# Performance work log

Measured on AMD Instinct MI355X. Metric: run time of the kernel, lower is better.

The kernel has to match this reference:

```python
import jax, jax.numpy as jnp
import numpy as np


def _quant(x, bits):
    # Symmetric per-tensor uniform quantization with straight-through rounding
    # (scale detached, as in typical QConv2d/QLinear low-bit implementations).
    n = 2.0 ** (bits - 1) - 1.0  # 7 levels each side for 4-bit
    s = jax.lax.stop_gradient(jnp.max(jnp.abs(x)) / n + 1e-8)
    q = jnp.clip(x / s, -n, n)
    q = q + jax.lax.stop_gradient(jnp.round(q) - q)  # STE round
    return q * s


def setup_inputs() -> dict:
    key = jax.random.key(0)
    k1, k2, k3, k4, k5 = jax.random.split(key, 5)
    B = 8192
    x = jax.random.normal(k1, (B, 1, 28, 28), dtype=jnp.float32)
    conv_w = jax.random.normal(k2, (16, 1, 3, 3), dtype=jnp.float32) * 0.1
    conv_b = jax.random.normal(k3, (16,), dtype=jnp.float32) * 0.01
    fc_w = jax.random.normal(k4, (10, 576), dtype=jnp.float32) * 0.05
    fc_b = jax.random.normal(k5, (10,), dtype=jnp.float32) * 0.01
    return {"x": x, "conv_w": conv_w, "conv_b": conv_b, "fc_w": fc_w, "fc_b": fc_b}


def reference(x, conv_w, conv_b, fc_w, fc_b):
    WBIT = 4
    ABIT = 4
    # QConv2d: quantize activations and weights to 4-bit, then conv (VALID, stride 1)
    xq = _quant(x, ABIT)
    wq = _quant(conv_w, WBIT)
    y = jax.lax.conv_general_dilated(
        xq, wq, window_strides=(1, 1), padding="VALID",
        dimension_numbers=("NCHW", "OIHW", "NCHW"))  # [B,16,26,26]
    y = y + conv_b[None, :, None, None]
    y = jax.nn.relu(y)
    # MaxPool2d(4): 4x4 window, stride 4 -> [B,16,6,6]
    y = jax.lax.reduce_window(y, -jnp.inf, jax.lax.max,
                              (1, 1, 4, 4), (1, 1, 4, 4), "VALID")
    flat = y.reshape(y.shape[0], -1)  # [B,576], channel-major like torch.flatten
    # QLinear: quantize activations and weights, then matmul
    fq = _quant(flat, ABIT)
    fwq = _quant(fc_w, WBIT)
    out = fq @ fwq.T + fc_b  # [B,10]
    return out
```

## Files before the change

kernel.cpp:

```cpp
#include <hip/hip_runtime.h>


#define DEV __device__ __forceinline__

DEV float quantq(float v, float s) {
  return rintf(fminf(7.0f, fmaxf(-7.0f, v / s)));
}

DEV float block_reduce_max(float v, float* smem) {
#pragma unroll
  for (int off = 32; off > 0; off >>= 1)
    v = fmaxf(v, __shfl_xor(v, off, 64));
  __syncthreads();
  if ((threadIdx.x & 63) == 0) smem[threadIdx.x >> 6] = v;
  __syncthreads();
  float m = smem[0];
  for (int i = 1; i < ((int)blockDim.x >> 6); ++i) m = fmaxf(m, smem[i]);
  return m;
}

__global__ __launch_bounds__(256) void prep_kernel(
    const float* __restrict__ cw, const float* __restrict__ fw,
    unsigned int* __restrict__ scal) {
  __shared__ float smem[8];
  const int tid = threadIdx.x;
  float m1 = 0.f;
  for (int i = tid; i < 144; i += 256) m1 = fmaxf(m1, fabsf(cw[i]));
  m1 = block_reduce_max(m1, smem);
  float m2 = 0.f;
  for (int i = tid; i < 5760; i += 256) m2 = fmaxf(m2, fabsf(fw[i]));
  m2 = block_reduce_max(m2, smem);
  if (tid == 0) {
    scal[0] = 0u;
    scal[1] = __float_as_uint(m1);
    scal[2] = __float_as_uint(m2);
    scal[3] = 0u;
  }
}

__global__ __launch_bounds__(256) void maxabs_x_kernel(
    const float4* __restrict__ x4, int n4, unsigned int* __restrict__ scal) {
  __shared__ float smem[8];
  float m = 0.f;
  for (int i = blockIdx.x * blockDim.x + threadIdx.x; i < n4;
       i += gridDim.x * blockDim.x) {
    float4 v = x4[i];
    m = fmaxf(m, fmaxf(fmaxf(fabsf(v.x), fabsf(v.y)),
                       fmaxf(fabsf(v.z), fabsf(v.w))));
  }
  m = block_reduce_max(m, smem);
  if (threadIdx.x == 0) atomicMax(scal + 0, __float_as_uint(m));
}

#define IMGS_PER_BLK 7
__global__ __launch_bounds__(256) void conv_pool_kernel(
    const float* __restrict__ x, const float* __restrict__ cw,
    const float* __restrict__ cb, unsigned int* __restrict__ scal,
    float* __restrict__ flat) {
  __shared__ __align__(16) float qx[IMGS_PER_BLK * 784];
  __shared__ float qw[16][9];
  __shared__ float bias[16];
  __shared__ float smem[8];
  const int tid = threadIdx.x;
  const int b0 = blockIdx.x * IMGS_PER_BLK;
  const int nimg = min(IMGS_PER_BLK, 8192 - b0);
  const float sx = __uint_as_float(scal[0]) / 7.0f + 1e-8f;
  const float sw = __uint_as_float(scal[1]) / 7.0f + 1e-8f;
  const float sxw = sx * sw;
  {
    const float4* x4 = (const float4*)x + b0 * 196;
    float4* q4 = (float4*)qx;
    const int n4 = nimg * 196;
    for (int i = tid; i < n4; i += 256) {
      float4 v = x4[i];
      float4 q;
      q.x = quantq(v.x, sx); q.y = quantq(v.y, sx);
      q.z = quantq(v.z, sx); q.w = quantq(v.w, sx);
      q4[i] = q;
    }
  }
  if (tid < 144) qw[tid / 9][tid % 9] = quantq(cw[tid], sw);
  if (tid < 16) bias[tid] = cb[tid];
  __syncthreads();
  float lmax = 0.f;
  if (tid < nimg * 36) {
    const int img = tid / 36, pp = tid % 36, pi = pp / 6, pj = pp % 6;
    const float* base = &qx[img * 784 + pi * 4 * 28 + pj * 4];
    float r[36];
#pragma unroll
    for (int rr = 0; rr < 6; ++rr)
#pragma unroll
      for (int cc = 0; cc < 6; ++cc) r[rr * 6 + cc] = base[rr * 28 + cc];
    float* fo = &flat[(b0 + img) * 576 + pp];
#pragma unroll
    for (int c = 0; c < 16; ++c) {
      const float w0 = qw[c][0], w1 = qw[c][1], w2 = qw[c][2];
      const float w3 = qw[c][3], w4 = qw[c][4], w5 = qw[c][5];
      const float w6 = qw[c][6], w7 = qw[c][7], w8 = qw[c][8];
      const float bc = bias[c];
      float m = 0.f;
#pragma unroll
      for (int dr = 0; dr < 4; ++dr)
#pragma unroll
        for (int dc = 0; dc < 4; ++dc) {
          const float* q = &r[dr * 6 + dc];
          float acc = q[0] * w0 + q[1] * w1 + q[2] * w2
                    + q[6] * w3 + q[7] * w4 + q[8] * w5
                    + q[12] * w6 + q[13] * w7 + q[14] * w8;
          m = fmaxf(m, acc * sxw + bc);
        }
      fo[c * 36] = m;
      lmax = fmaxf(lmax, m);
    }
  }
  lmax = block_reduce_max(lmax, smem);
  if (tid == 0) atomicMax(scal + 3, __float_as_uint(lmax));
}

__global__ __launch_bounds__(256) void fc_kernel(
    const float* __restrict__ flat, const float* __restrict__ fw,
    const float* __restrict__ fb, const unsigned int* __restrict__ scal,
    float* __restrict__ out) {
  __shared__ float qfw[5760];
  __shared__ float sb[10];
  const float sf = __uint_as_float(scal[3]) / 7.0f + 1e-8f;
  const float sfw = __uint_as_float(scal[2]) / 7.0f + 1e-8f;
  const int tid = threadIdx.x;
  for (int i = tid; i < 5760; i += 256) qfw[i] = quantq(fw[i], sfw);
  if (tid < 10) sb[tid] = fb[tid];
  __syncthreads();
  const int wave = tid >> 6, lane = tid & 63;
  const int b = blockIdx.x * 4 + wave;
  float acc[10];
#pragma unroll
  for (int o = 0; o < 10; ++o) acc[o] = 0.f;
  const float* frow = &flat[b * 576];
#pragma unroll
  for (int j = 0; j < 9; ++j) {
    const int k = j * 64 + lane;
    const float qf = quantq(frow[k], sf);
#pragma unroll
    for (int o = 0; o < 10; ++o) acc[o] += qf * qfw[o * 576 + k];
  }
#pragma unroll
  for (int o = 0; o < 10; ++o)
#pragma unroll
    for (int off = 32; off > 0; off >>= 1)
      acc[o] += __shfl_xor(acc[o], off, 64);
  if (lane == 0) {
    const float ss = sf * sfw;
#pragma unroll
    for (int o = 0; o < 10; ++o) out[b * 10 + o] = acc[o] * ss + sb[o];
  }
}

extern "C" void kernel_launch(void* const* d_in, const int* in_sizes, int n_in,
                              void* d_out, int out_size, void* d_ws, size_t ws_size,
                              hipStream_t stream) {
  const float* x  = (const float*)d_in[0];
  const float* cw = (const float*)d_in[1];
  const float* cb = (const float*)d_in[2];
  const float* fw = (const float*)d_in[3];
  const float* fb = (const float*)d_in[4];
  float* out = (float*)d_out;
  unsigned int* scal = (unsigned int*)d_ws;
  float* flat = (float*)((char*)d_ws + 256);

  prep_kernel<<<1, 256, 0, stream>>>(cw, fw, scal);
  maxabs_x_kernel<<<1024, 256, 0, stream>>>(
      (const float4*)x, (8192 * 784) / 4, scal);
  conv_pool_kernel<<<(8192 + IMGS_PER_BLK - 1) / IMGS_PER_BLK, 256, 0, stream>>>(
      x, cw, cb, scal, flat);
  fc_kernel<<<2048, 256, 0, stream>>>(flat, fw, fb, scal, out);
}
```

Before: 157.0 us.

## Fold weight max-abs into x reduction and parallelize conv over channels

Removes the separate single-block prep kernel by folding the conv and fc weight max-abs reductions into block 0 of the input max-abs kernel, with a memset to zero the scalars instead. The conv-pool kernel now processes one image per 576-thread block, one thread per (channel, pooled pixel), rather than 7 images per block with 36 threads looping over 16 channels. This aims to raise thread-level parallelism and coalesce the flat stores, at the cost of reloading input rows per channel from shared memory and more block scheduling overhead.

```diff
diff --git a/kernel.cpp b/kernel.cpp
--- a/kernel.cpp
+++ b/kernel.cpp
@@ -19,27 +19,9 @@
   return m;
 }
 
-__global__ __launch_bounds__(256) void prep_kernel(
-    const float* __restrict__ cw, const float* __restrict__ fw,
-    unsigned int* __restrict__ scal) {
-  __shared__ float smem[8];
-  const int tid = threadIdx.x;
-  float m1 = 0.f;
-  for (int i = tid; i < 144; i += 256) m1 = fmaxf(m1, fabsf(cw[i]));
-  m1 = block_reduce_max(m1, smem);
-  float m2 = 0.f;
-  for (int i = tid; i < 5760; i += 256) m2 = fmaxf(m2, fabsf(fw[i]));
-  m2 = block_reduce_max(m2, smem);
-  if (tid == 0) {
-    scal[0] = 0u;
-    scal[1] = __float_as_uint(m1);
-    scal[2] = __float_as_uint(m2);
-    scal[3] = 0u;
-  }
-}
-
-__global__ __launch_bounds__(256) void maxabs_x_kernel(
-    const float4* __restrict__ x4, int n4, unsigned int* __restrict__ scal) {
+__global__ __launch_bounds__(256) void maxabs_kernel(
+    const float4* __restrict__ x4, int n4, const float* __restrict__ cw,
+    const float* __restrict__ fw, unsigned int* __restrict__ scal) {
   __shared__ float smem[8];
   float m = 0.f;
   for (int i = blockIdx.x * blockDim.x + threadIdx.x; i < n4;
@@ -50,70 +32,74 @@
   }
   m = block_reduce_max(m, smem);
   if (threadIdx.x == 0) atomicMax(scal + 0, __float_as_uint(m));
+  if (blockIdx.x == 0) {
+    const int tid = threadIdx.x;
+    float m1 = 0.f;
+    for (int i = tid; i < 144; i += 256) m1 = fmaxf(m1, fabsf(cw[i]));
+    m1 = block_reduce_max(m1, smem);
+    float m2 = 0.f;
+    for (int i = tid; i < 5760; i += 256) m2 = fmaxf(m2, fabsf(fw[i]));
+    m2 = block_reduce_max(m2, smem);
+    if (tid == 0) {
+      scal[1] = __float_as_uint(m1);
+      scal[2] = __float_as_uint(m2);
+    }
+  }
 }
 
-#define IMGS_PER_BLK 7
-__global__ __launch_bounds__(256) void conv_pool_kernel(
+__global__ __launch_bounds__(576) void conv_pool_kernel(
     const float* __restrict__ x, const float* __restrict__ cw,
     const float* __restrict__ cb, unsigned int* __restrict__ scal,
     float* __restrict__ flat) {
-  __shared__ __align__(16) float qx[IMGS_PER_BLK * 784];
-  __shared__ float qw[16][9];
+  __shared__ __align__(16) float qx[784];
+  __shared__ float qw[144];
   __shared__ float bias[16];
-  __shared__ float smem[8];
+  __shared__ float smem[16];
   const int tid = threadIdx.x;
-  const int b0 = blockIdx.x * IMGS_PER_BLK;
-  const int nimg = min(IMGS_PER_BLK, 8192 - b0);
+  const int b = blockIdx.x;
   const float sx = __uint_as_float(scal[0]) / 7.0f + 1e-8f;
   const float sw = __uint_as_float(scal[1]) / 7.0f + 1e-8f;
   const float sxw = sx * sw;
-  {
-    const float4* x4 = (const float4*)x + b0 * 196;
-    float4* q4 = (float4*)qx;
-    const int n4 = nimg * 196;
-    for (int i = tid; i < n4; i += 256) {
-      float4 v = x4[i];
-      float4 q;
-      q.x = quantq(v.x, sx); q.y = quantq(v.y, sx);
-      q.z = quantq(v.z, sx); q.w = quantq(v.w, sx);
-      q4[i] = q;
+  if (tid < 196) {
+    float4 v = ((const float4*)x)[b * 196 + tid];
+    float4 q;
+    q.x = quantq(v.x, sx); q.y = quantq(v.y, sx);
+    q.z = quantq(v.z, sx); q.w = quantq(v.w, sx);
+    ((float4*)qx)[tid] = q;
+  } else if (tid < 340) {
+    const int i = tid - 196;
+    qw[i] = quantq(cw[i], sw);
+  } else if (tid < 356) {
+    bias[tid - 340] = cb[tid - 340];
+  }
+  __syncthreads();
+  const int c = tid / 36, pp = tid % 36, pi = pp / 6, pj = pp % 6;
+  float w[9];
+#pragma unroll
+  for (int i = 0; i < 9; ++i) w[i] = qw[c * 9 + i];
+  const float bc = bias[c];
+  const float* base = &qx[pi * 112 + pj * 4];
+  float r[36];
+#pragma unroll
+  for (int rr = 0; rr < 6; ++rr) {
+    const float4 v4 = *(const float4*)(base + rr * 28);
+    const float2 v2 = *(const float2*)(base + rr * 28 + 4);
+    r[rr * 6 + 0] = v4.x; r[rr * 6 + 1] = v4.y; r[rr * 6 + 2] = v4.z;
+    r[rr * 6 + 3] = v4.w; r[rr * 6 + 4] = v2.x; r[rr * 6 + 5] = v2.y;
+  }
+  float m = 0.f;
+#pragma unroll
+  for (int dr = 0; dr < 4; ++dr)
+#pragma unroll
+    for (int dc = 0; dc < 4; ++dc) {
+      const float* q = &r[dr * 6 + dc];
+      float acc = q[0] * w[0] + q[1] * w[1] + q[2] * w[2]
+                + q[6] * w[3] + q[7] * w[4] + q[8] * w[5]
+                + q[12] * w[6] + q[13] * w[7] + q[14] * w[8];
+      m = fmaxf(m, acc * sxw + bc);
     }
-  }
-  if (tid < 144) qw[tid / 9][tid % 9] = quantq(cw[tid], sw);
-  if (tid < 16) bias[tid] = cb[tid];
-  __syncthreads();
-  float lmax = 0.f;
-  if (tid < nimg * 36) {
-    const int img = tid / 36, pp = tid % 36, pi = pp / 6, pj = pp % 6;
-    const float* base = &qx[img * 784 + pi * 4 * 28 + pj * 4];
-    float r[36];
-#pragma unroll
-    for (int rr = 0; rr < 6; ++rr)
-#pragma unroll
-      for (int cc = 0; cc < 6; ++cc) r[rr * 6 + cc] = base[rr * 28 + cc];
-    float* fo = &flat[(b0 + img) * 576 + pp];
-#pragma unroll
-    for (int c = 0; c < 16; ++c) {
-      const float w0 = qw[c][0], w1 = qw[c][1], w2 = qw[c][2];
-      const float w3 = qw[c][3], w4 = qw[c][4], w5 = qw[c][5];
-      const float w6 = qw[c][6], w7 = qw[c][7], w8 = qw[c][8];
-      const float bc = bias[c];
-      float m = 0.f;
-#pragma unroll
-      for (int dr = 0; dr < 4; ++dr)
-#pragma unroll
-        for (int dc = 0; dc < 4; ++dc) {
-          const float* q = &r[dr * 6 + dc];
-          float acc = q[0] * w0 + q[1] * w1 + q[2] * w2
-                    + q[6] * w3 + q[7] * w4 + q[8] * w5
-                    + q[12] * w6 + q[13] * w7 + q[14] * w8;
-          m = fmaxf(m, acc * sxw + bc);
-        }
-      fo[c * 36] = m;
-      lmax = fmaxf(lmax, m);
-    }
-  }
-  lmax = block_reduce_max(lmax, smem);
+  flat[b * 576 + tid] = m;
+  float lmax = block_reduce_max(m, smem);
   if (tid == 0) atomicMax(scal + 3, __float_as_uint(lmax));
 }
 
@@ -166,10 +152,9 @@
   unsigned int* scal = (unsigned int*)d_ws;
   float* flat = (float*)((char*)d_ws + 256);
 
-  prep_kernel<<<1, 256, 0, stream>>>(cw, fw, scal);
-  maxabs_x_kernel<<<1024, 256, 0, stream>>>(
-      (const float4*)x, (8192 * 784) / 4, scal);
-  conv_pool_kernel<<<(8192 + IMGS_PER_BLK - 1) / IMGS_PER_BLK, 256, 0, stream>>>(
-      x, cw, cb, scal, flat);
+  hipMemsetAsync(scal, 0, 16, stream);
+  maxabs_kernel<<<2048, 256, 0, stream>>>(
+      (const float4*)x, (8192 * 784) / 4, cw, fw, scal);
+  conv_pool_kernel<<<8192, 576, 0, stream>>>(x, cw, cb, scal, flat);
   fc_kernel<<<2048, 256, 0, stream>>>(flat, fw, fb, scal, out);
 }
```

Result: slower. 215.7 us (+37.4%).
